# Kernel optimization log

Measured on AMD Instinct MI355X. Metric: run time of the kernel, lower is better.

Reference implementation:

```python
import jax, jax.numpy as jnp
import numpy as np

B, N, D = 2, 2048, 1024
H = 16
DH = D // H
SCALE = 1.0 / np.sqrt(D).astype(np.float32)  # faithful: module uses 1/sqrt(d_out), not head_dim


def setup_inputs() -> dict:
    key = jax.random.key(0)
    ks = jax.random.split(key, 5)
    s = 0.02
    return {
        "x": jax.random.normal(ks[0], (B, N, D), dtype=jnp.float32),
        "Wq": jax.random.normal(ks[1], (D, D), dtype=jnp.float32) * s,
        "Wk": jax.random.normal(ks[2], (D, D), dtype=jnp.float32) * s,
        "Wv": jax.random.normal(ks[3], (D, D), dtype=jnp.float32) * s,
        "Wo": jax.random.normal(ks[4], (D, D), dtype=jnp.float32) * s,
        "bo": jnp.zeros((D,), dtype=jnp.float32),
    }


def reference(x, Wq, Wk, Wv, Wo, bo):
    b, n, _ = x.shape
    # qkv projections (no bias), split heads: [b, H, n, DH]
    q = (x @ Wq).reshape(b, n, H, DH).transpose(0, 2, 1, 3)
    k = (x @ Wk).reshape(b, n, H, DH).transpose(0, 2, 1, 3)
    v = (x @ Wv).reshape(b, n, H, DH).transpose(0, 2, 1, 3)
    # full N x N scores (the module materializes this)
    scores = jnp.einsum("bhqd,bhkd->bhqk", q, k)
    causal = jnp.triu(jnp.ones((n, n), dtype=bool), k=1)  # True above diagonal -> masked
    scores = jnp.where(causal[None, None], -jnp.inf, scores)
    # faithful order: mask first, then scale, then softmax (-inf * scale stays -inf)
    attn = jax.nn.softmax(scores * SCALE, axis=-1)
    ctx = jnp.einsum("bhqk,bhkd->bhqd", attn, v)
    ctx = ctx.transpose(0, 2, 1, 3).reshape(b, n, D)
    return ctx @ Wo + bo
```

## Files before the change

kernel.cpp:

```cpp
#include <hip/hip_runtime.h>
#include <stdint.h>

#define H 16
#define DH 64
#define BATCH 2
#define NSEQ 2048
#define DMODEL 1024
#define QSZ (BATCH*H*NSEQ*DH)
#define ATT_CS 0.04508422017f

typedef __attribute__((ext_vector_type(8))) short short8;
typedef __attribute__((ext_vector_type(4))) short shortx4;
typedef __attribute__((ext_vector_type(4))) float floatx4;

__device__ __forceinline__ short f2bf(float f) {
  union { float f; unsigned u; } c; c.f = f;
  unsigned u = c.u;
  unsigned r = (u + 0x7FFFu + ((u >> 16) & 1u)) >> 16;
  return (short)r;
}

__device__ __forceinline__ unsigned pk2bf(float a, float b) {
  union { float f; unsigned u; } ca, cb; ca.f = a; cb.f = b;
  return __builtin_amdgcn_perm(cb.u + 0x8000u, ca.u + 0x8000u, 0x07060302u);
}

__device__ __forceinline__ void gld_lds16(const short* g, short* l) {
  __builtin_amdgcn_global_load_lds((const __attribute__((address_space(1))) unsigned int*)g,
                                   (__attribute__((address_space(3))) unsigned int*)l,
                                   16, 0, 0);
}

__global__ __launch_bounds__(256) void prep_kernel(const float* __restrict__ x,
                                                   const float* __restrict__ Wq,
                                                   const float* __restrict__ Wk,
                                                   const float* __restrict__ Wv,
                                                   const float* __restrict__ Wo,
                                                   short* __restrict__ xb,
                                                   short* __restrict__ wqkvt,
                                                   short* __restrict__ wot) {
  __shared__ short tile[32][33];
  int bid = blockIdx.x;
  if (bid < 4096) {
    int i = bid * 256 + threadIdx.x;
    float4 v = ((const float4*)x)[i];
    short4 o;
    o.x = f2bf(v.x); o.y = f2bf(v.y); o.z = f2bf(v.z); o.w = f2bf(v.w);
    ((short4*)xb)[i] = o;
  } else {
    int t = bid - 4096;
    int widx = t >> 10, rem = t & 1023;
    int bx = rem & 31, by = rem >> 5;
    const float* W = (widx == 0) ? Wq : (widx == 1) ? Wk : (widx == 2) ? Wv : Wo;
    short* dst = (widx < 3) ? (wqkvt + (size_t)widx * 1048576) : wot;
    int k0 = bx * 32, n0 = by * 32;
    int tx = threadIdx.x & 31, ty = threadIdx.x >> 5;
#pragma unroll
    for (int i = 0; i < 4; i++) {
      int k = k0 + ty + i * 8;
      tile[tx][ty + i * 8] = f2bf(W[(size_t)k * DMODEL + n0 + tx]);
    }
    __syncthreads();
#pragma unroll
    for (int i = 0; i < 4; i++) {
      int n = n0 + ty + i * 8;
      dst[(size_t)n * DMODEL + k0 + tx] = tile[ty + i * 8][tx];
    }
  }
}

template <int MODE, int NT>
__global__ __launch_bounds__(256) void gemm_bt(const short* __restrict__ A,
                                               const short* __restrict__ Bt,
                                               short* __restrict__ outb,
                                               float* __restrict__ outf,
                                               const float* __restrict__ bias,
                                               int K, int nbn) {
  constexpr int JF = NT / 32;
  __shared__ __align__(16) short As[2][4096];
  __shared__ __align__(16) short Bs[2][NT * 32];
  int tid = threadIdx.x;
  int lane = tid & 63;
  int w = tid >> 6;
  int wm = w >> 1, wn = w & 1;
  int m16 = lane & 15, quad = lane >> 4;
  int cpx = nbn >> 3;
  int xcd = blockIdx.x & 7, local = blockIdx.x >> 3;
  int bn = xcd * cpx + local % cpx;
  int bm = local / cpx;

  floatx4 acc[4][JF];
#pragma unroll
  for (int i = 0; i < 4; i++)
#pragma unroll
    for (int j = 0; j < JF; j++) acc[i][j] = (floatx4){0.f, 0.f, 0.f, 0.f};

  const short* Ablk = A + (size_t)bm * 128 * K;
  const short* Bblk = Bt + (size_t)bn * NT * K;

  auto stage = [&](int k0, int b) {
#pragma unroll
    for (int t = 0; t < 2; t++) {
      int e = w * 1024 + t * 512 + lane * 8;
      int row = e >> 5, col = e & 31;
      gld_lds16(Ablk + (size_t)row * K + k0 + col, &As[b][w * 1024 + t * 512]);
    }
    if constexpr (NT == 128) {
#pragma unroll
      for (int t = 0; t < 2; t++) {
        int e = w * 1024 + t * 512 + lane * 8;
        int row = e >> 5, col = e & 31;
        gld_lds16(Bblk + (size_t)row * K + k0 + col, &Bs[b][w * 1024 + t * 512]);
      }
    } else {
      int e = w * 512 + lane * 8;
      int row = e >> 5, col = e & 31;
      gld_lds16(Bblk + (size_t)row * K + k0 + col, &Bs[b][w * 512]);
    }
  };

  stage(0, 0);
  for (int k0 = 0; k0 < K; k0 += 32) {
    int b = (k0 >> 5) & 1;
    __syncthreads();
    short8 af[4], bfr[JF];
#pragma unroll
    for (int i = 0; i < 4; i++)
      af[i] = *(const short8*)&As[b][(wm * 64 + i * 16 + m16) * 32 + quad * 8];
#pragma unroll
    for (int j = 0; j < JF; j++)
      bfr[j] = *(const short8*)&Bs[b][(wn * (NT / 2) + j * 16 + m16) * 32 + quad * 8];
    if (k0 + 32 < K) stage(k0 + 32, b ^ 1);
#pragma unroll
    for (int i = 0; i < 4; i++)
#pragma unroll
      for (int j = 0; j < JF; j++)
        acc[i][j] = __builtin_amdgcn_mfma_f32_16x16x32_bf16(af[i], bfr[j], acc[i][j], 0, 0, 0);
  }

  if constexpr (MODE == 0) {
    int which0 = (bn * NT) >> 10;
    if (which0 == 2) {
#pragma unroll
      for (int i = 0; i < 4; i++) {
        int mrow_base = bm * 128 + wm * 64 + i * 16 + quad * 4;
        int b = mrow_base >> 11, ns0 = mrow_base & 2047;
#pragma unroll
        for (int j = 0; j < JF; j++) {
          int ncol = bn * NT + wn * (NT / 2) + j * 16 + m16;
          int c = ncol & 1023;
          int h = c >> 6, dh = c & 63;
          shortx4 pk;
#pragma unroll
          for (int r = 0; r < 4; r++) pk[r] = f2bf(acc[i][j][r]);
          *(shortx4*)&outb[2 * (size_t)QSZ + (((size_t)(b * H + h) * DH + dh) * NSEQ) + ns0] = pk;
        }
      }
    } else {
      __syncthreads();
      float sc = (which0 == 0) ? ATT_CS : 1.0f;
      float* tp = ((float*)&As[0][0]) + w * 1024;
#pragma unroll
      for (int i = 0; i < 4; i++) {
        int mrow = bm * 128 + wm * 64 + i * 16 + m16;
        int b = mrow >> 11, ns = mrow & 2047;
#pragma unroll
        for (int j = 0; j < JF; j++) {
          int cbase = (bn * NT + wn * (NT / 2) + j * 16) & 1023;
          int h = cbase >> 6, dhb = cbase & 63;
          *(floatx4*)&tp[m16 * 20 + quad * 4] = acc[i][j];
          shortx4 pk;
#pragma unroll
          for (int cc = 0; cc < 4; cc++)
            pk[cc] = f2bf(tp[(quad * 4 + cc) * 20 + m16] * sc);
          *(shortx4*)&outb[(size_t)which0 * QSZ +
                           ((size_t)(b * H + h) * NSEQ + ns) * DH + dhb + quad * 4] = pk;
        }
      }
    }
  } else {
#pragma unroll
    for (int i = 0; i < 4; i++) {
      int mrow_base = bm * 128 + wm * 64 + i * 16 + quad * 4;
#pragma unroll
      for (int j = 0; j < JF; j++) {
        int ncol = bn * NT + wn * (NT / 2) + j * 16 + m16;
#pragma unroll
        for (int r = 0; r < 4; r++)
          outf[(size_t)(mrow_base + r) * DMODEL + ncol] = acc[i][j][r] + bias[ncol];
      }
    }
  }
}

__global__ __launch_bounds__(256) void attn_kernel(const short* __restrict__ Qw,
                                                   const short* __restrict__ Kw,
                                                   const short* __restrict__ VtG,
                                                   short* __restrict__ ctx) {
  __shared__ __align__(16) short Ks[2][4096];
  __shared__ __align__(16) short Vt[2][4096];
  __shared__ __align__(16) short Ps[2][4][16 * 72];
  int id = blockIdx.x;
  int bh = (id & 7) + ((id >> 7) << 3);
  int bx = (id >> 3) & 15;
  int tid = threadIdx.x, lane = tid & 63, w = tid >> 6;
  int m16 = lane & 15, quad = lane >> 4;
  int sw = m16 & 7;
  const size_t base = (size_t)bh * NSEQ * DH;
  const short* Kg0 = Kw + base;
  const short* Vg0 = VtG + base;
  short* PwA = &Ps[0][w][0];
  short* PwB = &Ps[1][w][0];

  int qbA = bx;
  int qbB = 31 - bx;
  int q0A = qbA * 64 + w * 16;
  int q0B = qbB * 64 + w * 16;

  short8 qfA[2], qfB[2];
#pragma unroll
  for (int kk = 0; kk < 2; kk++) {
    qfA[kk] = *(const short8*)(Qw + base + (size_t)(q0A + m16) * DH + kk * 32 + quad * 8);
    qfB[kk] = *(const short8*)(Qw + base + (size_t)(q0B + m16) * DH + kk * 32 + quad * 8);
  }

  float lA = 0.f, lB = 0.f;
  floatx4 oA[4], oB[4];
#pragma unroll
  for (int d = 0; d < 4; d++) { oA[d] = (floatx4){0.f,0.f,0.f,0.f}; oB[d] = (floatx4){0.f,0.f,0.f,0.f}; }

  short8 kf[4][2], vf[4][2];

  auto stage = [&](int kc, int sub) {
#pragma unroll
    for (int t = 0; t < 2; t++) {
      int e = w * 1024 + t * 512 + lane * 8;
      int r = e >> 6;
      int g = ((e >> 3) & 7) ^ (r & 7);
      gld_lds16(Kg0 + (size_t)(kc * 64 + r) * DH + g * 8, &Ks[sub][w * 1024 + t * 512]);
      gld_lds16(Vg0 + (size_t)r * NSEQ + kc * 64 + g * 8, &Vt[sub][w * 1024 + t * 512]);
    }
  };

  auto tile_qk = [&](bool diag, int kc, int q0, const short8* qf,
                     float& l, short* Pw) {
    floatx4 st[4];
#pragma unroll
    for (int nj = 0; nj < 4; nj++) {
      floatx4 s = (floatx4){0.f, 0.f, 0.f, 0.f};
      s = __builtin_amdgcn_mfma_f32_16x16x32_bf16(kf[nj][0], qf[0], s, 0, 0, 0);
      s = __builtin_amdgcn_mfma_f32_16x16x32_bf16(kf[nj][1], qf[1], s, 0, 0, 0);
      st[nj] = s;
    }
    int qrow = q0 + m16;
    float sum = 0.f;
#pragma unroll
    for (int nj = 0; nj < 4; nj++) {
      float p0 = __builtin_amdgcn_exp2f(st[nj][0]);
      float p1 = __builtin_amdgcn_exp2f(st[nj][1]);
      float p2 = __builtin_amdgcn_exp2f(st[nj][2]);
      float p3 = __builtin_amdgcn_exp2f(st[nj][3]);
      if (diag) {
        int key = kc * 64 + nj * 16 + quad * 4;
        p0 = (key     <= qrow) ? p0 : 0.f;
        p1 = (key + 1 <= qrow) ? p1 : 0.f;
        p2 = (key + 2 <= qrow) ? p2 : 0.f;
        p3 = (key + 3 <= qrow) ? p3 : 0.f;
      }
      sum += (p0 + p1) + (p2 + p3);
      uint2 pk;
      pk.x = pk2bf(p0, p1);
      pk.y = pk2bf(p2, p3);
      *(uint2*)&Pw[m16 * 72 + nj * 16 + quad * 4] = pk;
    }
    sum += __shfl_xor(sum, 16, 64);
    sum += __shfl_xor(sum, 32, 64);
    l += sum;
  };

  auto tile_pv = [&](floatx4* o, const short* Pw) {
    short8 pf[2];
    pf[0] = *(const short8*)&Pw[m16 * 72 + quad * 8];
    pf[1] = *(const short8*)&Pw[m16 * 72 + 32 + quad * 8];
#pragma unroll
    for (int d = 0; d < 4; d++) {
#pragma unroll
      for (int kj = 0; kj < 2; kj++)
        o[d] = __builtin_amdgcn_mfma_f32_16x16x32_bf16(vf[d][kj], pf[kj], o[d], 0, 0, 0);
    }
  };

  for (int c0 = 0; c0 <= qbB; c0 += 2) {
    bool has2 = (c0 + 1 <= qbB);
    __syncthreads();
    stage(c0, 0);
    if (has2) stage(c0 + 1, 1);
    __syncthreads();
#pragma unroll
    for (int s = 0; s < 2; s++) {
      int kc = c0 + s;
      if (s == 1 && !has2) break;
#pragma unroll
      for (int nj = 0; nj < 4; nj++) {
        kf[nj][0] = *(const short8*)&Ks[s][(nj * 16 + m16) * 64 + ((quad ^ sw) * 8)];
        kf[nj][1] = *(const short8*)&Ks[s][(nj * 16 + m16) * 64 + (((4 + quad) ^ sw) * 8)];
      }
#pragma unroll
      for (int d = 0; d < 4; d++) {
        vf[d][0] = *(const short8*)&Vt[s][(d * 16 + m16) * 64 + ((quad ^ sw) * 8)];
        vf[d][1] = *(const short8*)&Vt[s][(d * 16 + m16) * 64 + (((4 + quad) ^ sw) * 8)];
      }
      if (kc <= qbA) {
        tile_qk(kc == qbA, kc, q0A, qfA, lA, PwA);
        tile_qk(false,     kc, q0B, qfB, lB, PwB);
        tile_pv(oA, PwA);
        tile_pv(oB, PwB);
      } else {
        tile_qk(kc == qbB, kc, q0B, qfB, lB, PwB);
        tile_pv(oB, PwB);
      }
    }
  }

  int b = bh >> 4, h = bh & 15;
#pragma unroll
  for (int s = 0; s < 2; s++) {
    int q0 = s ? q0B : q0A;
    float inv = 1.f / (s ? lB : lA);
    floatx4* o = s ? oB : oA;
    size_t rowbase = ((size_t)(b * NSEQ + q0 + m16)) * DMODEL + h * DH;
#pragma unroll
    for (int d = 0; d < 4; d++) {
      shortx4 pk;
#pragma unroll
      for (int r = 0; r < 4; r++) pk[r] = f2bf(o[d][r] * inv);
      *(shortx4*)&ctx[rowbase + d * 16 + quad * 4] = pk;
    }
  }
}

extern "C" void kernel_launch(void* const* d_in, const int* in_sizes, int n_in,
                              void* d_out, int out_size, void* d_ws, size_t ws_size,
                              hipStream_t stream) {
  const float* x  = (const float*)d_in[0];
  const float* Wq = (const float*)d_in[1];
  const float* Wk = (const float*)d_in[2];
  const float* Wv = (const float*)d_in[3];
  const float* Wo = (const float*)d_in[4];
  const float* bo = (const float*)d_in[5];
  float* out = (float*)d_out;

  char* ws = (char*)d_ws;
  short* xb    = (short*)(ws);
  short* wqkvt = (short*)(ws + (8ull << 20));
  short* wot   = (short*)(ws + (14ull << 20));
  short* qkvws = (short*)(ws + (16ull << 20));
  short* ctx   = (short*)(ws + (40ull << 20));

  prep_kernel<<<8192, 256, 0, stream>>>(x, Wq, Wk, Wv, Wo, xb, wqkvt, wot);

  gemm_bt<0, 128><<<32 * 24, 256, 0, stream>>>(xb, wqkvt, qkvws, nullptr, nullptr, 1024, 24);

  short* qws = qkvws;
  short* kws = qkvws + QSZ;
  short* vtg = qkvws + 2 * QSZ;
  attn_kernel<<<512, 256, 0, stream>>>(qws, kws, vtg, ctx);

  gemm_bt<1, 64><<<32 * 16, 256, 0, stream>>>(ctx, wot, nullptr, out, bo, 1024, 16);
}
```

Measured before the change: 179.5 us.

## Split attention key chunks across two wave groups with LDS reduction

The attention block grows from 4 to 8 waves. Two groups of four waves each handle alternate 64-key chunks of the same query tiles, with one chunk staged per group. At the end, group 1 writes its partial O and row sums to LDS and group 0 adds them and writes the output. This doubles the waves available to hide latency per block, at the cost of an extra reduction and syncthreads, and lower occupancy per thread because of the launch bound.

```diff
diff --git a/kernel.cpp b/kernel.cpp
--- a/kernel.cpp
+++ b/kernel.cpp
@@ -193,29 +193,29 @@
   }
 }
 
-__global__ __launch_bounds__(256) void attn_kernel(const short* __restrict__ Qw,
-                                                   const short* __restrict__ Kw,
-                                                   const short* __restrict__ VtG,
-                                                   short* __restrict__ ctx) {
+__global__ __launch_bounds__(512, 4) void attn_kernel(const short* __restrict__ Qw,
+                                                      const short* __restrict__ Kw,
+                                                      const short* __restrict__ VtG,
+                                                      short* __restrict__ ctx) {
   __shared__ __align__(16) short Ks[2][4096];
   __shared__ __align__(16) short Vt[2][4096];
-  __shared__ __align__(16) short Ps[2][4][16 * 72];
+  __shared__ __align__(16) short Ps[8][16 * 72];
   int id = blockIdx.x;
   int bh = (id & 7) + ((id >> 7) << 3);
   int bx = (id >> 3) & 15;
   int tid = threadIdx.x, lane = tid & 63, w = tid >> 6;
+  int grp = w >> 2, wl = w & 3;
   int m16 = lane & 15, quad = lane >> 4;
   int sw = m16 & 7;
   const size_t base = (size_t)bh * NSEQ * DH;
   const short* Kg0 = Kw + base;
   const short* Vg0 = VtG + base;
-  short* PwA = &Ps[0][w][0];
-  short* PwB = &Ps[1][w][0];
+  short* Pw = &Ps[w][0];
 
   int qbA = bx;
   int qbB = 31 - bx;
-  int q0A = qbA * 64 + w * 16;
-  int q0B = qbB * 64 + w * 16;
+  int q0A = qbA * 64 + wl * 16;
+  int q0B = qbB * 64 + wl * 16;
 
   short8 qfA[2], qfB[2];
 #pragma unroll
@@ -231,19 +231,18 @@
 
   short8 kf[4][2], vf[4][2];
 
-  auto stage = [&](int kc, int sub) {
+  auto stage = [&](int kc) {
 #pragma unroll
     for (int t = 0; t < 2; t++) {
-      int e = w * 1024 + t * 512 + lane * 8;
+      int e = wl * 1024 + t * 512 + lane * 8;
       int r = e >> 6;
-      int g = ((e >> 3) & 7) ^ (r & 7);
-      gld_lds16(Kg0 + (size_t)(kc * 64 + r) * DH + g * 8, &Ks[sub][w * 1024 + t * 512]);
-      gld_lds16(Vg0 + (size_t)r * NSEQ + kc * 64 + g * 8, &Vt[sub][w * 1024 + t * 512]);
+      int gb = ((e >> 3) & 7) ^ (r & 7);
+      gld_lds16(Kg0 + (size_t)(kc * 64 + r) * DH + gb * 8, &Ks[grp][wl * 1024 + t * 512]);
+      gld_lds16(Vg0 + (size_t)r * NSEQ + kc * 64 + gb * 8, &Vt[grp][wl * 1024 + t * 512]);
     }
   };
 
-  auto tile_qk = [&](bool diag, int kc, int q0, const short8* qf,
-                     float& l, short* Pw) {
+  auto tile_qk = [&](bool diag, int kc, int q0, const short8* qf, float& l) {
     floatx4 st[4];
 #pragma unroll
     for (int nj = 0; nj < 4; nj++) {
@@ -278,7 +277,7 @@
     l += sum;
   };
 
-  auto tile_pv = [&](floatx4* o, const short* Pw) {
+  auto tile_pv = [&](floatx4* o) {
     short8 pf[2];
     pf[0] = *(const short8*)&Pw[m16 * 72 + quad * 8];
     pf[1] = *(const short8*)&Pw[m16 * 72 + 32 + quad * 8];
@@ -291,50 +290,70 @@
   };
 
   for (int c0 = 0; c0 <= qbB; c0 += 2) {
-    bool has2 = (c0 + 1 <= qbB);
+    int kc = c0 + grp;
+    bool valid = kc <= qbB;
     __syncthreads();
-    stage(c0, 0);
-    if (has2) stage(c0 + 1, 1);
+    if (valid) stage(kc);
     __syncthreads();
+    if (!valid) continue;
+#pragma unroll
+    for (int nj = 0; nj < 4; nj++) {
+      kf[nj][0] = *(const short8*)&Ks[grp][(nj * 16 + m16) * 64 + ((quad ^ sw) * 8)];
+      kf[nj][1] = *(const short8*)&Ks[grp][(nj * 16 + m16) * 64 + (((4 + quad) ^ sw) * 8)];
+    }
+#pragma unroll
+    for (int d = 0; d < 4; d++) {
+      vf[d][0] = *(const short8*)&Vt[grp][(d * 16 + m16) * 64 + ((quad ^ sw) * 8)];
+      vf[d][1] = *(const short8*)&Vt[grp][(d * 16 + m16) * 64 + (((4 + quad) ^ sw) * 8)];
+    }
+    if (kc <= qbA) {
+      tile_qk(kc == qbA, kc, q0A, qfA, lA);
+      tile_pv(oA);
+      tile_qk(false,     kc, q0B, qfB, lB);
+      tile_pv(oB);
+    } else {
+      tile_qk(kc == qbB, kc, q0B, qfB, lB);
+      tile_pv(oB);
+    }
+  }
+
+  __syncthreads();
+  float* smA = (float*)&Ks[0][0];
+  float* smB = (float*)&Vt[0][0];
+  float* sl  = (float*)&Ps[0][0];
+  if (grp == 1) {
+#pragma unroll
+    for (int d = 0; d < 4; d++) {
+      *(floatx4*)&smA[(wl * 4 + d) * 256 + lane * 4] = oA[d];
+      *(floatx4*)&smB[(wl * 4 + d) * 256 + lane * 4] = oB[d];
+    }
+    sl[wl * 128 + lane] = lA;
+    sl[wl * 128 + 64 + lane] = lB;
+  }
+  __syncthreads();
+  if (grp == 0) {
+#pragma unroll
+    for (int d = 0; d < 4; d++) {
+      oA[d] += *(const floatx4*)&smA[(wl * 4 + d) * 256 + lane * 4];
+      oB[d] += *(const floatx4*)&smB[(wl * 4 + d) * 256 + lane * 4];
+    }
+    lA += sl[wl * 128 + lane];
+    lB += sl[wl * 128 + 64 + lane];
+
+    int b = bh >> 4, h = bh & 15;
 #pragma unroll
     for (int s = 0; s < 2; s++) {
-      int kc = c0 + s;
-      if (s == 1 && !has2) break;
-#pragma unroll
-      for (int nj = 0; nj < 4; nj++) {
-        kf[nj][0] = *(const short8*)&Ks[s][(nj * 16 + m16) * 64 + ((quad ^ sw) * 8)];
-        kf[nj][1] = *(const short8*)&Ks[s][(nj * 16 + m16) * 64 + (((4 + quad) ^ sw) * 8)];
-      }
+      int q0 = s ? q0B : q0A;
+      float inv = 1.f / (s ? lB : lA);
+      floatx4* o = s ? oB : oA;
+      size_t rowbase = ((size_t)(b * NSEQ + q0 + m16)) * DMODEL + h * DH;
 #pragma unroll
       for (int d = 0; d < 4; d++) {
-        vf[d][0] = *(const short8*)&Vt[s][(d * 16 + m16) * 64 + ((quad ^ sw) * 8)];
-        vf[d][1] = *(const short8*)&Vt[s][(d * 16 + m16) * 64 + (((4 + quad) ^ sw) * 8)];
-      }
-      if (kc <= qbA) {
-        tile_qk(kc == qbA, kc, q0A, qfA, lA, PwA);
-        tile_qk(false,     kc, q0B, qfB, lB, PwB);
-        tile_pv(oA, PwA);
-        tile_pv(oB, PwB);
-      } else {
-        tile_qk(kc == qbB, kc, q0B, qfB, lB, PwB);
-        tile_pv(oB, PwB);
-      }
-    }
-  }
-
-  int b = bh >> 4, h = bh & 15;
-#pragma unroll
-  for (int s = 0; s < 2; s++) {
-    int q0 = s ? q0B : q0A;
-    float inv = 1.f / (s ? lB : lA);
-    floatx4* o = s ? oB : oA;
-    size_t rowbase = ((size_t)(b * NSEQ + q0 + m16)) * DMODEL + h * DH;
-#pragma unroll
-    for (int d = 0; d < 4; d++) {
-      shortx4 pk;
-#pragma unroll
-      for (int r = 0; r < 4; r++) pk[r] = f2bf(o[d][r] * inv);
-      *(shortx4*)&ctx[rowbase + d * 16 + quad * 4] = pk;
+        shortx4 pk;
+#pragma unroll
+        for (int r = 0; r < 4; r++) pk[r] = f2bf(o[d][r] * inv);
+        *(shortx4*)&ctx[rowbase + d * 16 + quad * 4] = pk;
+      }
     }
   }
 }
@@ -364,7 +383,7 @@
   short* qws = qkvws;
   short* kws = qkvws + QSZ;
   short* vtg = qkvws + 2 * QSZ;
-  attn_kernel<<<512, 256, 0, stream>>>(qws, kws, vtg, ctx);
+  attn_kernel<<<512, 512, 0, stream>>>(qws, kws, vtg, ctx);
 
   gemm_bt<1, 64><<<32 * 16, 256, 0, stream>>>(ctx, wot, nullptr, out, bo, 1024, 16);
 }
```

Result: slower. 233.9 us (+30.3%).
